# Kernel tuning notes

Hardware: AMD Instinct MI355X
Metric: run time of the kernel (lower is better)

Reference implementation:

```python
import jax, jax.numpy as jnp
import numpy as np

D_MODEL = 1024
D_HIDDEN = 4096
NUM_EXPERTS = 8
K_ACTIVE = 2


def setup_inputs() -> dict:
    key = jax.random.key(0)
    ks = jax.random.split(key, 8)
    x = jax.random.normal(ks[0], (1, 2048, D_MODEL), dtype=jnp.float32)
    gate_w = jax.random.normal(ks[1], (D_MODEL, NUM_EXPERTS), dtype=jnp.float32) * 0.02
    gate_b = jnp.zeros((NUM_EXPERTS,), dtype=jnp.float32)
    w1 = jax.random.normal(ks[2], (NUM_EXPERTS, D_MODEL, D_HIDDEN), dtype=jnp.float32) * 0.02
    b1 = jnp.zeros((NUM_EXPERTS, D_HIDDEN), dtype=jnp.float32)
    w2 = jax.random.normal(ks[3], (NUM_EXPERTS, D_HIDDEN, D_MODEL), dtype=jnp.float32) * 0.02
    b2 = jnp.zeros((NUM_EXPERTS, D_MODEL), dtype=jnp.float32)
    return {"x": x, "gate_w": gate_w, "gate_b": gate_b,
            "w1": w1, "b1": b1, "w2": w2, "b2": b2}


def reference(x, gate_w, gate_b, w1, b1, w2, b2):
    B, S, D = x.shape
    xf = x.reshape(-1, D)                                    # [T, D]
    logits = xf @ gate_w + gate_b                            # [T, E]
    top_w, top_idx = jax.lax.top_k(logits, K_ACTIVE)         # [T, K]
    top_w = jax.nn.softmax(top_w, axis=-1)                   # softmax over selected experts
    # combine-weight per expert: sum over k slots of one-hot(idx) * weight -> [T, E]
    gates = jnp.sum(jax.nn.one_hot(top_idx, NUM_EXPERTS, dtype=xf.dtype) * top_w[..., None], axis=1)
    # expert FFN applied per expert (dropout is identity in eval): gelu is exact (erf), matching torch nn.GELU default
    h = jax.nn.gelu(jnp.einsum('td,edh->teh', xf, w1) + b1[None], approximate=False)  # [T, E, H]
    y = jnp.einsum('teh,ehd->ted', h, w2) + b2[None]         # [T, E, D]
    out = jnp.einsum('ted,te->td', y, gates)                 # weighted combine of selected experts
    return out.reshape(B, S, D)
```

## Files before the change

kernel.cpp:

```cpp
#include <hip/hip_runtime.h>
#include <stdint.h>

typedef unsigned short u16;
typedef __attribute__((ext_vector_type(8))) short s16x8;
typedef __attribute__((ext_vector_type(8))) u16  u16x8;
typedef __attribute__((ext_vector_type(4))) u16  u16x4;
typedef __attribute__((ext_vector_type(4))) float f32x4;

#define T_TOKENS 2048
#define DM 1024
#define DH 4096
#define NE 8
#define BM 128
#define BN 128
#define BN2 64
#define BK 64
#define MAXSLOTS (T_TOKENS*2 + NE*BM)
#define ROWBLK (MAXSLOTS/BM)

__device__ __forceinline__ u16 f2bf(float f) {
    union { float ff; uint32_t u; } v; v.ff = f;
    uint32_t r = v.u + 0x7fffu + ((v.u >> 16) & 1u);
    return (u16)(r >> 16);
}

#define GLOAD_LDS16(gsrc, ldst) \
    __builtin_amdgcn_global_load_lds((const __attribute__((address_space(1))) uint32_t*)(gsrc), \
                                     (__attribute__((address_space(3))) uint32_t*)(ldst), 16, 0, 0)

__global__ void k_convert(const float* __restrict__ x, u16* __restrict__ xbf,
                          int* __restrict__ ctrl) {
    int i = blockIdx.x * blockDim.x + threadIdx.x;
    const f32x4* xv = (const f32x4*)x;
    f32x4 a = xv[2*i], b = xv[2*i+1];
    u16x8 o;
    o[0]=f2bf(a[0]); o[1]=f2bf(a[1]); o[2]=f2bf(a[2]); o[3]=f2bf(a[3]);
    o[4]=f2bf(b[0]); o[5]=f2bf(b[1]); o[6]=f2bf(b[2]); o[7]=f2bf(b[3]);
    ((u16x8*)xbf)[i] = o;
    if (blockIdx.x == 0 && threadIdx.x < 32) ctrl[threadIdx.x] = 0;
}

__global__ void __launch_bounds__(256) k_transpose(const float* __restrict__ src,
                                                   u16* __restrict__ dst,
                                                   int K, int N) {
    __shared__ float tile[64][65];
    const int e = blockIdx.z;
    const int n0 = blockIdx.x * 64, k0 = blockIdx.y * 64;
    const float* s = src + (size_t)e * K * N;
    u16* d = dst + (size_t)e * K * N;
    const int tx = threadIdx.x & 15, ty = threadIdx.x >> 4;
    #pragma unroll
    for (int j = 0; j < 4; ++j) {
        int r = ty * 4 + j;
        f32x4 v = *(const f32x4*)(s + (size_t)(k0 + r) * N + n0 + tx * 4);
        tile[r][tx*4+0] = v[0]; tile[r][tx*4+1] = v[1];
        tile[r][tx*4+2] = v[2]; tile[r][tx*4+3] = v[3];
    }
    __syncthreads();
    #pragma unroll
    for (int j = 0; j < 4; ++j) {
        int n = ty * 4 + j;
        u16x4 w;
        #pragma unroll
        for (int c = 0; c < 4; ++c) w[c] = f2bf(tile[tx*4+c][n]);
        *(u16x4*)(d + (size_t)(n0 + n) * K + k0 + tx * 4) = w;
    }
}

__global__ void __launch_bounds__(64) k_gate(const float* __restrict__ x,
                                             const float* __restrict__ gw,
                                             const float* __restrict__ gb,
                                             int* __restrict__ cnt,
                                             int* __restrict__ tt_idx,
                                             float* __restrict__ tt_w) {
    const int t = blockIdx.x;
    const int lane = threadIdx.x;
    float acc[NE] = {0.f,0.f,0.f,0.f,0.f,0.f,0.f,0.f};
    const float* xr = x + (size_t)t * DM;
    #pragma unroll
    for (int c = 0; c < DM/64; ++c) {
        float xv = xr[lane + 64*c];
        const float* g = gw + (size_t)(lane + 64*c) * NE;
        #pragma unroll
        for (int e = 0; e < NE; ++e) acc[e] += xv * g[e];
    }
    #pragma unroll
    for (int e = 0; e < NE; ++e) {
        #pragma unroll
        for (int off = 32; off >= 1; off >>= 1)
            acc[e] += __shfl_xor(acc[e], off, 64);
    }
    if (lane == 0) {
        float l[NE];
        #pragma unroll
        for (int e = 0; e < NE; ++e) l[e] = acc[e] + gb[e];
        int i0 = 0;
        #pragma unroll
        for (int e = 1; e < NE; ++e) if (l[e] > l[i0]) i0 = e;
        int i1 = (i0 == 0) ? 1 : 0;
        #pragma unroll
        for (int e = 0; e < NE; ++e) if (e != i0 && l[e] > l[i1]) i1 = e;
        float m  = l[i0];
        float w0 = expf(l[i0] - m), w1 = expf(l[i1] - m);
        float s = w0 + w1; w0 /= s; w1 /= s;
        tt_idx[t*2] = i0; tt_idx[t*2+1] = i1;
        tt_w[t*2] = w0;  tt_w[t*2+1] = w1;
        atomicAdd(&cnt[i0], 1); atomicAdd(&cnt[i1], 1);
    }
}

__global__ void k_offsets(const int* __restrict__ cnt, int* __restrict__ fill,
                          int* __restrict__ off) {
    if (threadIdx.x == 0 && blockIdx.x == 0) {
        int a = 0;
        for (int e = 0; e < NE; ++e) {
            off[e] = a;
            a += (cnt[e] + BM - 1) / BM * BM;
            fill[e] = 0;
        }
        off[NE] = a;
    }
}

__global__ void k_scatter(const int* __restrict__ tt_idx, const float* __restrict__ tt_w,
                          const int* __restrict__ off, int* __restrict__ fill,
                          int* __restrict__ slot_token, float* __restrict__ slot_gate) {
    int t = blockIdx.x * blockDim.x + threadIdx.x;
    if (t >= T_TOKENS) return;
    #pragma unroll
    for (int k = 0; k < 2; ++k) {
        int e = tt_idx[t*2+k];
        int pos = off[e] + atomicAdd(&fill[e], 1);
        slot_token[pos] = t;
        slot_gate[pos]  = tt_w[t*2+k];
    }
}


__global__ void __launch_bounds__(256) k_ffn1_b16(
    const u16* __restrict__ xbf, const u16* __restrict__ w1t,
    const float* __restrict__ b1, const int* __restrict__ slot_token,
    const int* __restrict__ off, u16* __restrict__ h)
{
    __shared__ u16 As[BM*BK];
    __shared__ u16 Bs[BN*BK];
    const int rb = blockIdx.y, cb = blockIdx.x;
    const int total = off[NE];
    const int r0 = rb * BM;
    if (r0 >= total) return;
    int e = 0;
    while (e < NE-1 && off[e+1] <= r0) e++;
    const u16* Bsrc = w1t + (size_t)e * DM * DH;
    const float* be = b1 + (size_t)e * DH;

    const int tid = threadIdx.x;
    const int lane = tid & 63, wid = tid >> 6;
    const int wr = wid >> 1, wc = wid & 1;

    const u16* gA[4]; const u16* gB[4];
    #pragma unroll
    for (int i = 0; i < 4; ++i) {
        int row = wid*32 + i*8 + (lane >> 3);
        int g = (lane & 7) ^ (row & 7);
        int tok = slot_token[r0 + row];
        gA[i] = xbf + (size_t)tok * DM + g*8;
        gB[i] = Bsrc + (size_t)(cb*BN + row) * DM + g*8;
    }

    f32x4 acc[4][4];
    #pragma unroll
    for (int m = 0; m < 4; ++m)
        #pragma unroll
        for (int n = 0; n < 4; ++n) acc[m][n] = (f32x4){0.f,0.f,0.f,0.f};

    for (int kt = 0; kt < DM/BK; ++kt) {
        #pragma unroll
        for (int i = 0; i < 4; ++i) {
            GLOAD_LDS16(gA[i] + kt*BK, &As[(wid*32 + i*8)*BK]);
            GLOAD_LDS16(gB[i] + kt*BK, &Bs[(wid*32 + i*8)*BK]);
        }
        __syncthreads();
        #pragma unroll
        for (int ko = 0; ko < 2; ++ko) {
            s16x8 af[4], bfr[4];
            #pragma unroll
            for (int m = 0; m < 4; ++m) {
                int row = wr*64 + m*16 + (lane & 15);
                int sl = (ko*4 + (lane >> 4)) ^ (row & 7);
                af[m] = *(const s16x8*)&As[row*BK + sl*8];
            }
            #pragma unroll
            for (int n = 0; n < 4; ++n) {
                int col = wc*64 + n*16 + (lane & 15);
                int sl = (ko*4 + (lane >> 4)) ^ (col & 7);
                bfr[n] = *(const s16x8*)&Bs[col*BK + sl*8];
            }
            #pragma unroll
            for (int m = 0; m < 4; ++m)
                #pragma unroll
                for (int n = 0; n < 4; ++n)
                    acc[m][n] = __builtin_amdgcn_mfma_f32_16x16x32_bf16(af[m], bfr[n], acc[m][n], 0, 0, 0);
        }
        __syncthreads();
    }
    #pragma unroll
    for (int n = 0; n < 4; ++n) {
        int col = cb*BN + wc*64 + n*16 + (lane & 15);
        float bb = be[col];
        #pragma unroll
        for (int m = 0; m < 4; ++m) {
            int rbase = r0 + wr*64 + m*16 + (lane >> 4)*4;
            #pragma unroll
            for (int i = 0; i < 4; ++i) {
                float v = acc[m][n][i] + bb;
                float gv = 0.5f * v * (1.0f + erff(v * 0.70710678118654752f));
                h[(size_t)(rbase + i)*DH + col] = f2bf(gv);
            }
        }
    }
}

__global__ void __launch_bounds__(256) k_ffn2_b16(
    const u16* __restrict__ h, const u16* __restrict__ w2t,
    const float* __restrict__ b2, const int* __restrict__ slot_token,
    const float* __restrict__ slot_gate, const int* __restrict__ off,
    float* __restrict__ out)
{
    __shared__ u16 As[BM*BK];
    __shared__ u16 Bs[BN2*BK];
    const int rb = blockIdx.y, cb = blockIdx.x;
    const int total = off[NE];
    const int r0 = rb * BM;
    if (r0 >= total) return;
    int e = 0;
    while (e < NE-1 && off[e+1] <= r0) e++;
    const u16* Bsrc = w2t + (size_t)e * DH * DM;
    const float* be = b2 + (size_t)e * DM;

    const int tid = threadIdx.x;
    const int lane = tid & 63, wid = tid >> 6;
    const int wr = wid >> 1, wc = wid & 1;

    const u16* gA[4]; const u16* gB[2];
    #pragma unroll
    for (int i = 0; i < 4; ++i) {
        int row = wid*32 + i*8 + (lane >> 3);
        int g = (lane & 7) ^ (row & 7);
        gA[i] = h + (size_t)(r0 + row) * DH + g*8;
    }
    #pragma unroll
    for (int i = 0; i < 2; ++i) {
        int n = wid*16 + i*8 + (lane >> 3);
        int g = (lane & 7) ^ (n & 7);
        gB[i] = Bsrc + (size_t)(cb*BN2 + n) * DH + g*8;
    }

    f32x4 acc[4][2];
    #pragma unroll
    for (int m = 0; m < 4; ++m)
        #pragma unroll
        for (int n = 0; n < 2; ++n) acc[m][n] = (f32x4){0.f,0.f,0.f,0.f};

    for (int kt = 0; kt < DH/BK; ++kt) {
        #pragma unroll
        for (int i = 0; i < 4; ++i)
            GLOAD_LDS16(gA[i] + kt*BK, &As[(wid*32 + i*8)*BK]);
        #pragma unroll
        for (int i = 0; i < 2; ++i)
            GLOAD_LDS16(gB[i] + kt*BK, &Bs[(wid*16 + i*8)*BK]);
        __syncthreads();
        #pragma unroll
        for (int ko = 0; ko < 2; ++ko) {
            s16x8 af[4], bfr[2];
            #pragma unroll
            for (int m = 0; m < 4; ++m) {
                int row = wr*64 + m*16 + (lane & 15);
                int sl = (ko*4 + (lane >> 4)) ^ (row & 7);
                af[m] = *(const s16x8*)&As[row*BK + sl*8];
            }
            #pragma unroll
            for (int n = 0; n < 2; ++n) {
                int col = wc*32 + n*16 + (lane & 15);
                int sl = (ko*4 + (lane >> 4)) ^ (col & 7);
                bfr[n] = *(const s16x8*)&Bs[col*BK + sl*8];
            }
            #pragma unroll
            for (int m = 0; m < 4; ++m)
                #pragma unroll
                for (int n = 0; n < 2; ++n)
                    acc[m][n] = __builtin_amdgcn_mfma_f32_16x16x32_bf16(af[m], bfr[n], acc[m][n], 0, 0, 0);
        }
        __syncthreads();
    }
    float bb[2];
    #pragma unroll
    for (int n = 0; n < 2; ++n) bb[n] = be[cb*BN2 + wc*32 + n*16 + (lane & 15)];
    #pragma unroll
    for (int m = 0; m < 4; ++m) {
        #pragma unroll
        for (int i = 0; i < 4; ++i) {
            int s = r0 + wr*64 + m*16 + (lane >> 4)*4 + i;
            int tok = slot_token[s];
            float g = slot_gate[s];
            if (g != 0.0f) {
                float* orow = out + (size_t)tok * DM + cb*BN2 + wc*32;
                #pragma unroll
                for (int n = 0; n < 2; ++n)
                    atomicAdd(orow + n*16 + (lane & 15), g * (acc[m][n][i] + bb[n]));
            }
        }
    }
}


__global__ void __launch_bounds__(256) k_ffn1_f32(
    const u16* __restrict__ xbf, const float* __restrict__ w1,
    const float* __restrict__ b1, const int* __restrict__ slot_token,
    const int* __restrict__ off, u16* __restrict__ h)
{
    __shared__ u16 As[BM*BK];
    __shared__ u16 Bs[BN*BK];
    const int rb = blockIdx.y, cb = blockIdx.x;
    const int total = off[NE];
    const int r0 = rb * BM;
    if (r0 >= total) return;
    int e = 0;
    while (e < NE-1 && off[e+1] <= r0) e++;
    const float* Bsrc = w1 + (size_t)e * DM * DH;
    const float* be   = b1 + (size_t)e * DH;

    const int tid = threadIdx.x;
    const int lane = tid & 63, wid = tid >> 6;
    const int wr = wid >> 1, wc = wid & 1;

    const u16* gA[4];
    #pragma unroll
    for (int i = 0; i < 4; ++i) {
        int row = wid*32 + i*8 + (lane >> 3);
        int g = (lane & 7) ^ (row & 7);
        int tok = slot_token[r0 + row];
        gA[i] = xbf + (size_t)tok * DM + g*8;
    }
    const int tc = tid & 31, tr = tid >> 5;
    const float* gB = Bsrc + (size_t)(tr*8) * DH + cb*BN + tc*4;

    f32x4 acc[4][4];
    #pragma unroll
    for (int m = 0; m < 4; ++m)
        #pragma unroll
        for (int n = 0; n < 4; ++n) acc[m][n] = (f32x4){0.f,0.f,0.f,0.f};

    for (int kt = 0; kt < DM/BK; ++kt) {
        #pragma unroll
        for (int i = 0; i < 4; ++i)
            GLOAD_LDS16(gA[i] + kt*BK, &As[(wid*32 + i*8)*BK]);
        f32x4 bv[8];
        #pragma unroll
        for (int j = 0; j < 8; ++j)
            bv[j] = *(const f32x4*)(gB + (size_t)(kt*BK + j) * DH);
        #pragma unroll
        for (int c = 0; c < 4; ++c) {
            int n = tc*4 + c;
            int sl = tr ^ (n & 7);
            s16x8 pk;
            #pragma unroll
            for (int j = 0; j < 8; ++j) pk[j] = (short)f2bf(bv[j][c]);
            *(s16x8*)&Bs[n*BK + sl*8] = pk;
        }
        __syncthreads();
        #pragma unroll
        for (int ko = 0; ko < 2; ++ko) {
            s16x8 af[4], bfr[4];
            #pragma unroll
            for (int m = 0; m < 4; ++m) {
                int row = wr*64 + m*16 + (lane & 15);
                int sl = (ko*4 + (lane >> 4)) ^ (row & 7);
                af[m] = *(const s16x8*)&As[row*BK + sl*8];
            }
            #pragma unroll
            for (int n = 0; n < 4; ++n) {
                int col = wc*64 + n*16 + (lane & 15);
                int sl = (ko*4 + (lane >> 4)) ^ (col & 7);
                bfr[n] = *(const s16x8*)&Bs[col*BK + sl*8];
            }
            #pragma unroll
            for (int m = 0; m < 4; ++m)
                #pragma unroll
                for (int n = 0; n < 4; ++n)
                    acc[m][n] = __builtin_amdgcn_mfma_f32_16x16x32_bf16(af[m], bfr[n], acc[m][n], 0, 0, 0);
        }
        __syncthreads();
    }
    #pragma unroll
    for (int n = 0; n < 4; ++n) {
        int col = cb*BN + wc*64 + n*16 + (lane & 15);
        float bb = be[col];
        #pragma unroll
        for (int m = 0; m < 4; ++m) {
            int rbase = r0 + wr*64 + m*16 + (lane >> 4)*4;
            #pragma unroll
            for (int i = 0; i < 4; ++i) {
                float v = acc[m][n][i] + bb;
                float gv = 0.5f * v * (1.0f + erff(v * 0.70710678118654752f));
                h[(size_t)(rbase + i)*DH + col] = f2bf(gv);
            }
        }
    }
}

__global__ void __launch_bounds__(256) k_ffn2_f32(
    const u16* __restrict__ h, const float* __restrict__ w2,
    const float* __restrict__ b2, const int* __restrict__ slot_token,
    const float* __restrict__ slot_gate, const int* __restrict__ off,
    float* __restrict__ out)
{
    __shared__ u16 As[BM*BK];
    __shared__ u16 Bs[BN*BK];
    const int rb = blockIdx.y, cb = blockIdx.x;
    const int total = off[NE];
    const int r0 = rb * BM;
    if (r0 >= total) return;
    int e = 0;
    while (e < NE-1 && off[e+1] <= r0) e++;
    const float* Bsrc = w2 + (size_t)e * DH * DM;
    const float* be   = b2 + (size_t)e * DM;

    const int tid = threadIdx.x;
    const int lane = tid & 63, wid = tid >> 6;
    const int wr = wid >> 1, wc = wid & 1;

    const u16* gA[4];
    #pragma unroll
    for (int i = 0; i < 4; ++i) {
        int row = wid*32 + i*8 + (lane >> 3);
        int g = (lane & 7) ^ (row & 7);
        gA[i] = h + (size_t)(r0 + row) * DH + g*8;
    }
    const int tc = tid & 31, tr = tid >> 5;
    const float* gB = Bsrc + (size_t)(tr*8) * DM + cb*BN + tc*4;

    f32x4 acc[4][4];
    #pragma unroll
    for (int m = 0; m < 4; ++m)
        #pragma unroll
        for (int n = 0; n < 4; ++n) acc[m][n] = (f32x4){0.f,0.f,0.f,0.f};

    for (int kt = 0; kt < DH/BK; ++kt) {
        #pragma unroll
        for (int i = 0; i < 4; ++i)
            GLOAD_LDS16(gA[i] + kt*BK, &As[(wid*32 + i*8)*BK]);
        f32x4 bv[8];
        #pragma unroll
        for (int j = 0; j < 8; ++j)
            bv[j] = *(const f32x4*)(gB + (size_t)(kt*BK + j) * DM);
        #pragma unroll
        for (int c = 0; c < 4; ++c) {
            int n = tc*4 + c;
            int sl = tr ^ (n & 7);
            s16x8 pk;
            #pragma unroll
            for (int j = 0; j < 8; ++j) pk[j] = (short)f2bf(bv[j][c]);
            *(s16x8*)&Bs[n*BK + sl*8] = pk;
        }
        __syncthreads();
        #pragma unroll
        for (int ko = 0; ko < 2; ++ko) {
            s16x8 af[4], bfr[4];
            #pragma unroll
            for (int m = 0; m < 4; ++m) {
                int row = wr*64 + m*16 + (lane & 15);
                int sl = (ko*4 + (lane >> 4)) ^ (row & 7);
                af[m] = *(const s16x8*)&As[row*BK + sl*8];
            }
            #pragma unroll
            for (int n = 0; n < 4; ++n) {
                int col = wc*64 + n*16 + (lane & 15);
                int sl = (ko*4 + (lane >> 4)) ^ (col & 7);
                bfr[n] = *(const s16x8*)&Bs[col*BK + sl*8];
            }
            #pragma unroll
            for (int m = 0; m < 4; ++m)
                #pragma unroll
                for (int n = 0; n < 4; ++n)
                    acc[m][n] = __builtin_amdgcn_mfma_f32_16x16x32_bf16(af[m], bfr[n], acc[m][n], 0, 0, 0);
        }
        __syncthreads();
    }
    float bb[4];
    #pragma unroll
    for (int n = 0; n < 4; ++n) bb[n] = be[cb*BN + wc*64 + n*16 + (lane & 15)];
    #pragma unroll
    for (int m = 0; m < 4; ++m) {
        #pragma unroll
        for (int i = 0; i < 4; ++i) {
            int s = r0 + wr*64 + m*16 + (lane >> 4)*4 + i;
            int tok = slot_token[s];
            float g = slot_gate[s];
            if (g != 0.0f) {
                float* orow = out + (size_t)tok * DM + cb*BN + wc*64;
                #pragma unroll
                for (int n = 0; n < 4; ++n)
                    atomicAdd(orow + n*16 + (lane & 15), g * (acc[m][n][i] + bb[n]));
            }
        }
    }
}

extern "C" void kernel_launch(void* const* d_in, const int* in_sizes, int n_in,
                              void* d_out, int out_size, void* d_ws, size_t ws_size,
                              hipStream_t stream)
{
    (void)in_sizes; (void)n_in; (void)out_size;
    const float* x  = (const float*)d_in[0];
    const float* gw = (const float*)d_in[1];
    const float* gb = (const float*)d_in[2];
    const float* w1 = (const float*)d_in[3];
    const float* b1 = (const float*)d_in[4];
    const float* w2 = (const float*)d_in[5];
    const float* b2 = (const float*)d_in[6];
    float* out = (float*)d_out;
    char* ws = (char*)d_ws;

    const size_t OFF_XBF = 0;
    const size_t OFF_H   = 4194304;
    const size_t OFF_WT  = OFF_H + (size_t)MAXSLOTS * DH * 2;
    const size_t OFF_ST  = OFF_WT + (size_t)NE * DM * DH * 2;
    const size_t OFF_SG  = OFF_ST + MAXSLOTS * 4;
    const size_t OFF_TI  = OFF_SG + MAXSLOTS * 4;
    const size_t OFF_TW  = OFF_TI + T_TOKENS * 2 * 4;
    const size_t OFF_CT  = OFF_TW + T_TOKENS * 2 * 4;
    const size_t NEED_B16 = OFF_CT + 128;

    if (ws_size >= NEED_B16) {
        u16*   xbf        = (u16*)(ws + OFF_XBF);
        u16*   h          = (u16*)(ws + OFF_H);
        u16*   wt         = (u16*)(ws + OFF_WT);
        int*   slot_token = (int*)(ws + OFF_ST);
        float* slot_gate  = (float*)(ws + OFF_SG);
        int*   tt_idx     = (int*)(ws + OFF_TI);
        float* tt_w       = (float*)(ws + OFF_TW);
        int*   ctrl       = (int*)(ws + OFF_CT);
        int* cnt = ctrl; int* fill = ctrl + 8; int* offs = ctrl + 16;

        hipMemsetAsync(slot_token, 0, 2 * MAXSLOTS * 4, stream);
        hipMemsetAsync(out, 0, (size_t)T_TOKENS * DM * sizeof(float), stream);

        k_convert<<<(T_TOKENS*DM/8 + 255)/256, 256, 0, stream>>>(x, xbf, ctrl);
        k_gate<<<T_TOKENS, 64, 0, stream>>>(x, gw, gb, cnt, tt_idx, tt_w);
        k_offsets<<<1, 64, 0, stream>>>(cnt, fill, offs);
        k_scatter<<<(T_TOKENS + 255)/256, 256, 0, stream>>>(tt_idx, tt_w, offs, fill, slot_token, slot_gate);

        k_transpose<<<dim3(DH/64, DM/64, NE), 256, 0, stream>>>(w1, wt, DM, DH);
        k_ffn1_b16<<<dim3(DH/BN, ROWBLK), 256, 0, stream>>>(xbf, wt, b1, slot_token, offs, h);
        k_transpose<<<dim3(DM/64, DH/64, NE), 256, 0, stream>>>(w2, wt, DH, DM);
        k_ffn2_b16<<<dim3(DM/BN2, ROWBLK), 256, 0, stream>>>(h, wt, b2, slot_token, slot_gate, offs, out);
    } else {
        u16*   xbf        = (u16*)(ws);
        u16*   h          = (u16*)(ws + 4194304);
        int*   slot_token = (int*)(ws + 46137344);
        float* slot_gate  = (float*)(ws + 46157824);
        int*   tt_idx     = (int*)(ws + 46178304);
        float* tt_w       = (float*)(ws + 46194688);
        int*   ctrl       = (int*)(ws + 46211072);
        int* cnt = ctrl; int* fill = ctrl + 8; int* offs = ctrl + 16;

        hipMemsetAsync(slot_token, 0, 2 * MAXSLOTS * 4, stream);
        hipMemsetAsync(out, 0, (size_t)T_TOKENS * DM * sizeof(float), stream);

        k_convert<<<(T_TOKENS*DM/8 + 255)/256, 256, 0, stream>>>(x, xbf, ctrl);
        k_gate<<<T_TOKENS, 64, 0, stream>>>(x, gw, gb, cnt, tt_idx, tt_w);
        k_offsets<<<1, 64, 0, stream>>>(cnt, fill, offs);
        k_scatter<<<(T_TOKENS + 255)/256, 256, 0, stream>>>(tt_idx, tt_w, offs, fill, slot_token, slot_gate);
        k_ffn1_f32<<<dim3(DH/BN, ROWBLK), 256, 0, stream>>>(xbf, w1, b1, slot_token, offs, h);
        k_ffn2_f32<<<dim3(DM/BN, ROWBLK), 256, 0, stream>>>(h, w2, b2, slot_token, slot_gate, offs, out);
    }
}
```

Baseline: 311.8 us.

## Double-buffer LDS tiles in bf16 expert GEMM kernels to overlap loads with MFMA

Converts the k_ffn1_b16 and k_ffn2_b16 main loops to a two-stage LDS ping-pong. The next K tile is issued via direct global-to-LDS loads while MFMAs run on the current buffer, with one barrier per tile instead of two. The aim is to hide global load latency behind compute. This doubles LDS use per block, which may reduce occupancy. The other kernels only get their MFMA inner loop factored into a shared helper.

```diff
diff --git a/kernel.cpp b/kernel.cpp
--- a/kernel.cpp
+++ b/kernel.cpp
@@ -136,14 +136,64 @@
     }
 }
 
+__device__ __forceinline__ void mma64(const u16* As, const u16* Bs, int lane,
+                                      int wr, int wc, f32x4 acc[4][4]) {
+    #pragma unroll
+    for (int ko = 0; ko < 2; ++ko) {
+        s16x8 af[4], bfr[4];
+        #pragma unroll
+        for (int m = 0; m < 4; ++m) {
+            int row = wr*64 + m*16 + (lane & 15);
+            int sl = (ko*4 + (lane >> 4)) ^ (row & 7);
+            af[m] = *(const s16x8*)&As[row*BK + sl*8];
+        }
+        #pragma unroll
+        for (int n = 0; n < 4; ++n) {
+            int col = wc*64 + n*16 + (lane & 15);
+            int sl = (ko*4 + (lane >> 4)) ^ (col & 7);
+            bfr[n] = *(const s16x8*)&Bs[col*BK + sl*8];
+        }
+        #pragma unroll
+        for (int m = 0; m < 4; ++m)
+            #pragma unroll
+            for (int n = 0; n < 4; ++n)
+                acc[m][n] = __builtin_amdgcn_mfma_f32_16x16x32_bf16(af[m], bfr[n], acc[m][n], 0, 0, 0);
+    }
+}
+
+__device__ __forceinline__ void mma64_n2(const u16* As, const u16* Bs, int lane,
+                                         int wr, int wc, f32x4 acc[4][2]) {
+    #pragma unroll
+    for (int ko = 0; ko < 2; ++ko) {
+        s16x8 af[4], bfr[2];
+        #pragma unroll
+        for (int m = 0; m < 4; ++m) {
+            int row = wr*64 + m*16 + (lane & 15);
+            int sl = (ko*4 + (lane >> 4)) ^ (row & 7);
+            af[m] = *(const s16x8*)&As[row*BK + sl*8];
+        }
+        #pragma unroll
+        for (int n = 0; n < 2; ++n) {
+            int col = wc*32 + n*16 + (lane & 15);
+            int sl = (ko*4 + (lane >> 4)) ^ (col & 7);
+            bfr[n] = *(const s16x8*)&Bs[col*BK + sl*8];
+        }
+        #pragma unroll
+        for (int m = 0; m < 4; ++m)
+            #pragma unroll
+            for (int n = 0; n < 2; ++n)
+                acc[m][n] = __builtin_amdgcn_mfma_f32_16x16x32_bf16(af[m], bfr[n], acc[m][n], 0, 0, 0);
+    }
+}
+
 
 __global__ void __launch_bounds__(256) k_ffn1_b16(
     const u16* __restrict__ xbf, const u16* __restrict__ w1t,
     const float* __restrict__ b1, const int* __restrict__ slot_token,
     const int* __restrict__ off, u16* __restrict__ h)
 {
-    __shared__ u16 As[BM*BK];
-    __shared__ u16 Bs[BN*BK];
+    __shared__ u16 As[2][BM*BK];
+    __shared__ u16 Bs[2][BN*BK];
     const int rb = blockIdx.y, cb = blockIdx.x;
     const int total = off[NE];
     const int r0 = rb * BM;
@@ -173,36 +223,28 @@
         #pragma unroll
         for (int n = 0; n < 4; ++n) acc[m][n] = (f32x4){0.f,0.f,0.f,0.f};
 
-    for (int kt = 0; kt < DM/BK; ++kt) {
-        #pragma unroll
-        for (int i = 0; i < 4; ++i) {
-            GLOAD_LDS16(gA[i] + kt*BK, &As[(wid*32 + i*8)*BK]);
-            GLOAD_LDS16(gB[i] + kt*BK, &Bs[(wid*32 + i*8)*BK]);
-        }
-        __syncthreads();
-        #pragma unroll
-        for (int ko = 0; ko < 2; ++ko) {
-            s16x8 af[4], bfr[4];
-            #pragma unroll
-            for (int m = 0; m < 4; ++m) {
-                int row = wr*64 + m*16 + (lane & 15);
-                int sl = (ko*4 + (lane >> 4)) ^ (row & 7);
-                af[m] = *(const s16x8*)&As[row*BK + sl*8];
-            }
-            #pragma unroll
-            for (int n = 0; n < 4; ++n) {
-                int col = wc*64 + n*16 + (lane & 15);
-                int sl = (ko*4 + (lane >> 4)) ^ (col & 7);
-                bfr[n] = *(const s16x8*)&Bs[col*BK + sl*8];
-            }
-            #pragma unroll
-            for (int m = 0; m < 4; ++m)
-                #pragma unroll
-                for (int n = 0; n < 4; ++n)
-                    acc[m][n] = __builtin_amdgcn_mfma_f32_16x16x32_bf16(af[m], bfr[n], acc[m][n], 0, 0, 0);
-        }
-        __syncthreads();
-    }
+    #define STAGE1(buf, kt) do {                                              \
+        _Pragma("unroll")                                                     \
+        for (int i = 0; i < 4; ++i) {                                         \
+            GLOAD_LDS16(gA[i] + (kt)*BK, &As[buf][(wid*32 + i*8)*BK]);        \
+            GLOAD_LDS16(gB[i] + (kt)*BK, &Bs[buf][(wid*32 + i*8)*BK]);        \
+        }                                                                     \
+    } while (0)
+
+    const int NT = DM / BK;
+    STAGE1(0, 0);
+    __syncthreads();
+    #pragma unroll 1
+    for (int kt = 0; kt < NT; kt += 2) {
+        STAGE1(1, kt + 1);
+        mma64(As[0], Bs[0], lane, wr, wc, acc);
+        __syncthreads();
+        if (kt + 2 < NT) STAGE1(0, kt + 2);
+        mma64(As[1], Bs[1], lane, wr, wc, acc);
+        __syncthreads();
+    }
+    #undef STAGE1
+
     #pragma unroll
     for (int n = 0; n < 4; ++n) {
         int col = cb*BN + wc*64 + n*16 + (lane & 15);
@@ -226,8 +268,8 @@
     const float* __restrict__ slot_gate, const int* __restrict__ off,
     float* __restrict__ out)
 {
-    __shared__ u16 As[BM*BK];
-    __shared__ u16 Bs[BN2*BK];
+    __shared__ u16 As[2][BM*BK];
+    __shared__ u16 Bs[2][BN2*BK];
     const int rb = blockIdx.y, cb = blockIdx.x;
     const int total = off[NE];
     const int r0 = rb * BM;
@@ -261,37 +303,29 @@
         #pragma unroll
         for (int n = 0; n < 2; ++n) acc[m][n] = (f32x4){0.f,0.f,0.f,0.f};
 
-    for (int kt = 0; kt < DH/BK; ++kt) {
-        #pragma unroll
-        for (int i = 0; i < 4; ++i)
-            GLOAD_LDS16(gA[i] + kt*BK, &As[(wid*32 + i*8)*BK]);
-        #pragma unroll
-        for (int i = 0; i < 2; ++i)
-            GLOAD_LDS16(gB[i] + kt*BK, &Bs[(wid*16 + i*8)*BK]);
-        __syncthreads();
-        #pragma unroll
-        for (int ko = 0; ko < 2; ++ko) {
-            s16x8 af[4], bfr[2];
-            #pragma unroll
-            for (int m = 0; m < 4; ++m) {
-                int row = wr*64 + m*16 + (lane & 15);
-                int sl = (ko*4 + (lane >> 4)) ^ (row & 7);
-                af[m] = *(const s16x8*)&As[row*BK + sl*8];
-            }
-            #pragma unroll
-            for (int n = 0; n < 2; ++n) {
-                int col = wc*32 + n*16 + (lane & 15);
-                int sl = (ko*4 + (lane >> 4)) ^ (col & 7);
-                bfr[n] = *(const s16x8*)&Bs[col*BK + sl*8];
-            }
-            #pragma unroll
-            for (int m = 0; m < 4; ++m)
-                #pragma unroll
-                for (int n = 0; n < 2; ++n)
-                    acc[m][n] = __builtin_amdgcn_mfma_f32_16x16x32_bf16(af[m], bfr[n], acc[m][n], 0, 0, 0);
-        }
-        __syncthreads();
-    }
+    #define STAGE2(buf, kt) do {                                              \
+        _Pragma("unroll")                                                     \
+        for (int i = 0; i < 4; ++i)                                           \
+            GLOAD_LDS16(gA[i] + (kt)*BK, &As[buf][(wid*32 + i*8)*BK]);        \
+        _Pragma("unroll")                                                     \
+        for (int i = 0; i < 2; ++i)                                           \
+            GLOAD_LDS16(gB[i] + (kt)*BK, &Bs[buf][(wid*16 + i*8)*BK]);        \
+    } while (0)
+
+    const int NT = DH / BK;
+    STAGE2(0, 0);
+    __syncthreads();
+    #pragma unroll 1
+    for (int kt = 0; kt < NT; kt += 2) {
+        STAGE2(1, kt + 1);
+        mma64_n2(As[0], Bs[0], lane, wr, wc, acc);
+        __syncthreads();
+        if (kt + 2 < NT) STAGE2(0, kt + 2);
+        mma64_n2(As[1], Bs[1], lane, wr, wc, acc);
+        __syncthreads();
+    }
+    #undef STAGE2
+
     float bb[2];
     #pragma unroll
     for (int n = 0; n < 2; ++n) bb[n] = be[cb*BN2 + wc*32 + n*16 + (lane & 15)];
@@ -368,27 +402,7 @@
             *(s16x8*)&Bs[n*BK + sl*8] = pk;
         }
         __syncthreads();
-        #pragma unroll
-        for (int ko = 0; ko < 2; ++ko) {
-            s16x8 af[4], bfr[4];
-            #pragma unroll
-            for (int m = 0; m < 4; ++m) {
-                int row = wr*64 + m*16 + (lane & 15);
-                int sl = (ko*4 + (lane >> 4)) ^ (row & 7);
-                af[m] = *(const s16x8*)&As[row*BK + sl*8];
-            }
-            #pragma unroll
-            for (int n = 0; n < 4; ++n) {
-                int col = wc*64 + n*16 + (lane & 15);
-                int sl = (ko*4 + (lane >> 4)) ^ (col & 7);
-                bfr[n] = *(const s16x8*)&Bs[col*BK + sl*8];
-            }
-            #pragma unroll
-            for (int m = 0; m < 4; ++m)
-                #pragma unroll
-                for (int n = 0; n < 4; ++n)
-                    acc[m][n] = __builtin_amdgcn_mfma_f32_16x16x32_bf16(af[m], bfr[n], acc[m][n], 0, 0, 0);
-        }
+        mma64(As, Bs, lane, wr, wc, acc);
         __syncthreads();
     }
     #pragma unroll
@@ -463,27 +477,7 @@
             *(s16x8*)&Bs[n*BK + sl*8] = pk;
         }
         __syncthreads();
-        #pragma unroll
-        for (int ko = 0; ko < 2; ++ko) {
-            s16x8 af[4], bfr[4];
-            #pragma unroll
-            for (int m = 0; m < 4; ++m) {
-                int row = wr*64 + m*16 + (lane & 15);
-                int sl = (ko*4 + (lane >> 4)) ^ (row & 7);
-                af[m] = *(const s16x8*)&As[row*BK + sl*8];
-            }
-            #pragma unroll
-            for (int n = 0; n < 4; ++n) {
-                int col = wc*64 + n*16 + (lane & 15);
-                int sl = (ko*4 + (lane >> 4)) ^ (col & 7);
-                bfr[n] = *(const s16x8*)&Bs[col*BK + sl*8];
-            }
-            #pragma unroll
-            for (int m = 0; m < 4; ++m)
-                #pragma unroll
-                for (int n = 0; n < 4; ++n)
-                    acc[m][n] = __builtin_amdgcn_mfma_f32_16x16x32_bf16(af[m], bfr[n], acc[m][n], 0, 0, 0);
-        }
+        mma64(As, Bs, lane, wr, wc, acc);
         __syncthreads();
     }
     float bb[4];
```

Result: slower. 322.9 us (+3.6%).
